# Kernel optimization log

Hardware: AMD Instinct MI355X
Metric: run time of the kernel (lower is better)

Reference implementation:

```python
import jax, jax.numpy as jnp
import numpy as np

N_CHANNELS = 1024
N_HEADS = 16
SEQ = 2048
BATCH = 2


def setup_inputs() -> dict:
    key = jax.random.key(0)
    k1, k2, k3 = jax.random.split(key, 3)
    x = jax.random.normal(k1, (BATCH, SEQ, N_CHANNELS), dtype=jnp.float32)
    qkv_w = jax.random.normal(k2, (3 * N_CHANNELS, N_CHANNELS), dtype=jnp.float32) * 0.02
    qkv_b = jnp.zeros((3 * N_CHANNELS,), dtype=jnp.float32)
    proj_w = jax.random.normal(k3, (N_CHANNELS, N_CHANNELS), dtype=jnp.float32) * 0.02
    proj_b = jnp.zeros((N_CHANNELS,), dtype=jnp.float32)
    return {"x": x, "qkv_w": qkv_w, "qkv_b": qkv_b, "proj_w": proj_w, "proj_b": proj_b}


def reference(x, qkv_w, qkv_b, proj_w, proj_b):
    bs, t, c = x.shape
    h = N_HEADS
    hd = c // h
    scale = hd ** (-0.5)
    # qkv projection: torch Linear is x @ W^T + b
    qkv = x @ qkv_w.T + qkv_b  # [B, T, 3C]
    qkv = qkv.reshape(bs, t, 3, h, hd)
    q, k, v = qkv[:, :, 0], qkv[:, :, 1], qkv[:, :, 2]  # each [B, T, H, hd]
    logits = jnp.einsum('bthc,bshc->bhts', q, k) * scale  # [B, H, T, T]
    # causal mask: log(tril(ones)) -> 0 below diag, -inf above
    causal = jnp.tril(jnp.ones((t, t), dtype=bool))
    logits = jnp.where(causal[None, None], logits, -jnp.inf)
    attn = jax.nn.softmax(logits, axis=-1)
    out = jnp.einsum('bhts,bshc->bthc', attn, v).reshape(bs, t, c)
    out = out @ proj_w.T + proj_b
    return out
```

## Files before the change

### kernel.cpp

```cpp
#include <hip/hip_runtime.h>

typedef __bf16 bf16x8 __attribute__((ext_vector_type(8)));
typedef float f32x4 __attribute__((ext_vector_type(4)));
typedef float f32x16 __attribute__((ext_vector_type(16)));

__device__ inline ushort f2bf(float f) {
    unsigned u = __builtin_bit_cast(unsigned, f);
    unsigned r = (u + 0x7FFFu + ((u >> 16) & 1u)) >> 16;
    return (ushort)r;
}
__device__ inline float bf2f(ushort u) {
    unsigned x = ((unsigned)u) << 16;
    return __builtin_bit_cast(float, x);
}
__device__ inline uint4 pack8(const float* f) {
    uint4 r;
    r.x = (unsigned)f2bf(f[0]) | ((unsigned)f2bf(f[1]) << 16);
    r.y = (unsigned)f2bf(f[2]) | ((unsigned)f2bf(f[3]) << 16);
    r.z = (unsigned)f2bf(f[4]) | ((unsigned)f2bf(f[5]) << 16);
    r.w = (unsigned)f2bf(f[6]) | ((unsigned)f2bf(f[7]) << 16);
    return r;
}
__device__ inline unsigned cvtpk_bf16(float lo, float hi) {
    unsigned r;
    asm("v_cvt_pk_bf16_f32 %0, %1, %2" : "=v"(r) : "v"(lo), "v"(hi));
    return r;
}

#define MFMA_BF16(a, b, c) __builtin_amdgcn_mfma_f32_16x16x32_bf16(a, b, c, 0, 0, 0)
#define MFMA32(a, b, c) __builtin_amdgcn_mfma_f32_32x32x16_bf16(a, b, c, 0, 0, 0)
#define GLDS(g, l) __builtin_amdgcn_global_load_lds( \
    (const __attribute__((address_space(1))) void*)(g), \
    (__attribute__((address_space(3))) void*)(l), 16, 0, 0)

#define QSCALE 0.18033688011112042f

__global__ __launch_bounds__(256) void convert3(
    const float* __restrict__ s0, ushort* __restrict__ d0,
    const float* __restrict__ s1, ushort* __restrict__ d1,
    const float* __restrict__ s2, ushort* __restrict__ d2)
{
    const int i = blockIdx.x * 256 + threadIdx.x;
    const float* s; ushort* d; int off;
    if (i < 524288)      { s = s0; d = d0; off = i; }
    else if (i < 917504) { s = s1; d = d1; off = i - 524288; }
    else                 { s = s2; d = d2; off = i - 917504; }
    const float4* f = (const float4*)s + off * 2;
    float fa[8];
    *(float4*)&fa[0] = f[0];
    *(float4*)&fa[4] = f[1];
    ((uint4*)d)[off] = pack8(fa);
}

__global__ __launch_bounds__(256) void gemm_qkv(
    const ushort* __restrict__ A, const ushort* __restrict__ B,
    const float* __restrict__ bias,
    ushort* __restrict__ outQ, ushort* __restrict__ outK, ushort* __restrict__ outV,
    int N, int K)
{
    __shared__ __align__(16) ushort SMEM[32768];

    const int tid = threadIdx.x;
    const int w = tid >> 6;
    const int lane = tid & 63;
    const int l15 = lane & 15;
    const int quad = lane >> 4;
    const int srow = lane >> 3;

    const int bid = blockIdx.x + (blockIdx.y << 5);
    const int nb = (bid & 7) * 96 + (bid >> 3);
    const int m0 = (nb / 24) * 128;
    const int n0 = (nb % 24) * 128;
    const int wr = (w & 1) * 64;
    const int wc = (w >> 1) * 64;

    auto stage = [&](int k0, int buf) {
        ushort* As = SMEM + buf * 16384;
        ushort* Bs = As + 8192;
#pragma unroll
        for (int j = 0; j < 4; j++) {
            const int r0 = w * 32 + j * 8;
            const int row = r0 + srow;
            const int gcol = ((lane & 7) ^ (row & 7)) * 8;
            GLDS(A + (size_t)(m0 + row) * K + k0 + gcol, As + r0 * 64);
            GLDS(B + (size_t)(n0 + row) * K + k0 + gcol, Bs + r0 * 64);
        }
    };

    f32x4 acc[4][4] = {};

    stage(0, 0);
    __syncthreads();

    for (int k0 = 0; k0 < K; k0 += 64) {
        const int cur = (k0 >> 6) & 1;
        if (k0 + 64 < K) stage(k0 + 64, cur ^ 1);

        const ushort* As = SMEM + cur * 16384;
        const ushort* Bs = As + 8192;
        bf16x8 af[4][2], bf[4][2];
#pragma unroll
        for (int i = 0; i < 4; i++)
#pragma unroll
            for (int kk = 0; kk < 2; kk++) {
                const int ra = wr + i * 16 + l15;
                const int rb = wc + i * 16 + l15;
                af[i][kk] = *(const bf16x8*)&As[ra * 64 + (((kk * 4 + quad) ^ (ra & 7)) * 8)];
                bf[i][kk] = *(const bf16x8*)&Bs[rb * 64 + (((kk * 4 + quad) ^ (rb & 7)) * 8)];
            }
#pragma unroll
        for (int kk = 0; kk < 2; kk++)
#pragma unroll
            for (int mi = 0; mi < 4; mi++)
#pragma unroll
                for (int ni = 0; ni < 4; ni++)
                    acc[mi][ni] = MFMA_BF16(af[mi][kk], bf[ni][kk], acc[mi][ni]);
        __syncthreads();
    }

    const int which = n0 >> 10;
    ushort* Ct = SMEM;
    if (which == 2) {
#pragma unroll
        for (int mi = 0; mi < 4; mi++)
#pragma unroll
            for (int ni = 0; ni < 4; ni++)
#pragma unroll
                for (int r = 0; r < 4; r++) {
                    const int m_loc = wr + mi * 16 + quad * 4 + r;
                    const int n_loc = wc + ni * 16 + l15;
                    Ct[n_loc * 136 + m_loc] =
                        f2bf(acc[mi][ni][r] + bias[n0 + n_loc]);
                }
        __syncthreads();
        const int b = m0 >> 11;
#pragma unroll
        for (int i = 0; i < 8; i++) {
            const int vi = tid + i * 256;
            const int n_loc = vi >> 4, mblk = vi & 15;
            const uint4 val = *(const uint4*)&Ct[n_loc * 136 + mblk * 8];
            const int t = (m0 & 2047) + mblk * 8;
            const int c = (n0 + n_loc) & 1023;
            const int h = c >> 6, d = c & 63;
            *(uint4*)&outV[((size_t)(b * 16 + h) * 64 + d) * 2048 + t] = val;
        }
    } else {
        const float qs = (which == 0) ? QSCALE : 1.0f;
#pragma unroll
        for (int mi = 0; mi < 4; mi++)
#pragma unroll
            for (int ni = 0; ni < 4; ni++)
#pragma unroll
                for (int r = 0; r < 4; r++) {
                    const int m_loc = wr + mi * 16 + quad * 4 + r;
                    const int n_loc = wc + ni * 16 + l15;
                    Ct[m_loc * 136 + n_loc] =
                        f2bf((acc[mi][ni][r] + bias[n0 + n_loc]) * qs);
                }
        __syncthreads();
        ushort* outP = (which == 0) ? outQ : outK;
        const int hb = (n0 & 1023) >> 6;
        const int b = m0 >> 11;
#pragma unroll
        for (int i = 0; i < 8; i++) {
            const int vi = tid + i * 256;
            const int m_loc = vi >> 4, u = vi & 15;
            const uint4 val = *(const uint4*)&Ct[m_loc * 136 + u * 8];
            const int t = (m0 & 2047) + m_loc;
            const int h = hb + (u >> 3);
            const int d8 = (u & 7) * 8;
            *(uint4*)&outP[((size_t)(b * 16 + h)) * 131072 + (size_t)t * 64 + d8] = val;
        }
    }
}

__global__ __launch_bounds__(256) void gemm_proj(
    const ushort* __restrict__ A, const ushort* __restrict__ B,
    const float* __restrict__ bias, float* __restrict__ outD)
{
    const int N = 1024, K = 1024;
    __shared__ __align__(16) ushort SMEM[24576];

    const int tid = threadIdx.x;
    const int w = tid >> 6;
    const int lane = tid & 63;
    const int l15 = lane & 15;
    const int quad = lane >> 4;
    const int srow = lane >> 3;

    const int bid = blockIdx.x + (blockIdx.y << 6);
    const int nb = (bid & 7) * 64 + (bid >> 3);
    const int m0 = (nb >> 3) * 64;
    const int n0 = (nb & 7) * 128;
    const int wr = (w & 1) * 32;
    const int wc = (w >> 1) * 64;

    auto stage = [&](int k0, int buf) {
        ushort* As = SMEM + buf * 12288;
        ushort* Bs = As + 4096;
#pragma unroll
        for (int j = 0; j < 2; j++) {
            const int r0 = w * 16 + j * 8;
            const int row = r0 + srow;
            const int gcol = ((lane & 7) ^ (row & 7)) * 8;
            GLDS(A + (size_t)(m0 + row) * K + k0 + gcol, As + r0 * 64);
        }
#pragma unroll
        for (int j = 0; j < 4; j++) {
            const int r0 = w * 32 + j * 8;
            const int row = r0 + srow;
            const int gcol = ((lane & 7) ^ (row & 7)) * 8;
            GLDS(B + (size_t)(n0 + row) * K + k0 + gcol, Bs + r0 * 64);
        }
    };

    f32x4 acc[2][4] = {};

    stage(0, 0);
    __syncthreads();

    for (int k0 = 0; k0 < K; k0 += 64) {
        const int cur = (k0 >> 6) & 1;
        if (k0 + 64 < K) stage(k0 + 64, cur ^ 1);

        const ushort* As = SMEM + cur * 12288;
        const ushort* Bs = As + 4096;
        bf16x8 af[2][2], bf[4][2];
#pragma unroll
        for (int kk = 0; kk < 2; kk++) {
#pragma unroll
            for (int mi = 0; mi < 2; mi++) {
                const int ra = wr + mi * 16 + l15;
                af[mi][kk] = *(const bf16x8*)&As[ra * 64 + (((kk * 4 + quad) ^ (ra & 7)) * 8)];
            }
#pragma unroll
            for (int ni = 0; ni < 4; ni++) {
                const int rb = wc + ni * 16 + l15;
                bf[ni][kk] = *(const bf16x8*)&Bs[rb * 64 + (((kk * 4 + quad) ^ (rb & 7)) * 8)];
            }
        }
#pragma unroll
        for (int kk = 0; kk < 2; kk++)
#pragma unroll
            for (int mi = 0; mi < 2; mi++)
#pragma unroll
                for (int ni = 0; ni < 4; ni++)
                    acc[mi][ni] = MFMA_BF16(af[mi][kk], bf[ni][kk], acc[mi][ni]);
        __syncthreads();
    }

    float* Cf = (float*)SMEM;
#pragma unroll
    for (int cch = 0; cch < 2; cch++) {
        __syncthreads();
        if ((wc >> 6) == cch) {
#pragma unroll
            for (int mi = 0; mi < 2; mi++)
#pragma unroll
                for (int ni = 0; ni < 4; ni++)
#pragma unroll
                    for (int r = 0; r < 4; r++) {
                        const int m_loc = wr + mi * 16 + quad * 4 + r;
                        const int nl = ni * 16 + l15;
                        Cf[m_loc * 68 + nl] = acc[mi][ni][r] + bias[n0 + cch * 64 + nl];
                    }
        }
        __syncthreads();
#pragma unroll
        for (int i = 0; i < 4; i++) {
            const int vi = tid + i * 256;
            const int m_loc = vi >> 4, u = vi & 15;
            const float4 val = *(const float4*)&Cf[m_loc * 68 + u * 4];
            *(float4*)&outD[(size_t)(m0 + m_loc) * N + n0 + cch * 64 + u * 4] = val;
        }
    }
}

__global__ __launch_bounds__(256, 4) void attn_split(
    const ushort* __restrict__ Q, const ushort* __restrict__ K,
    const ushort* __restrict__ Vt, ushort* __restrict__ O,
    ushort* __restrict__ Opart, float* __restrict__ Lpart)
{
    __shared__ __align__(16) ushort KV[2][2][64 * 64];

    const int bid0 = blockIdx.x + blockIdx.y * 32;
    const int nb = (bid0 & 7) * 160 + (bid0 >> 3);
    const int bh = (nb / 160) * 4 + (nb % 160) / 40;
    const int y = nb % 40;

    int qt, k0, k1, split;
    const int slot = y - 4;
    if (y < 4) {
        qt = y; k0 = 0; k1 = 2 * qt + 2; split = 0;
    } else {
        split = 1;
        const int z = y - 4;
        int ci, c;
        if (z < 8)       { qt = 4 + (z >> 1); ci = z & 1; c = 2; }
        else if (z < 20) { const int t = z - 8;  qt = 8 + t / 3;   ci = t % 3; c = 3; }
        else             { const int t = z - 20; qt = 12 + (t >> 2); ci = t & 3; c = 4; }
        const int n = 2 * qt + 2;
        k0 = ci * n / c;
        k1 = (ci + 1) * n / c;
    }
    const int q0 = qt * 128;
    const int tid = threadIdx.x;
    const int w = tid >> 6;
    const int lane = tid & 63;
    const int l31 = lane & 31;
    const int hf = lane >> 5;
    const int wrow0 = q0 + w * 32;
    const int rowg = wrow0 + l31;

    auto stage = [&](int kt, int b) {
        const int t0 = kt * 64;
#pragma unroll
        for (int j = 0; j < 2; j++) {
            const int r0 = w * 16 + j * 8;
            const int row = r0 + (lane >> 3);
            const int gcol = ((lane & 7) ^ (row & 7)) * 8;
            GLDS(K + ((size_t)bh * 2048 + t0 + row) * 64 + gcol, &KV[b][0][r0 * 64]);
            GLDS(Vt + ((size_t)bh * 64 + row) * 2048 + t0 + gcol, &KV[b][1][r0 * 64]);
        }
    };

    const ushort* qbase = Q + ((size_t)bh * 2048 + rowg) * 64 + hf * 8;
    bf16x8 qf[4];
#pragma unroll
    for (int db = 0; db < 4; db++) qf[db] = *(const bf16x8*)(qbase + db * 16);

    bf16x8 ones;
#pragma unroll
    for (int j = 0; j < 8; j++) ones[j] = (__bf16)1.0f;

    f32x16 oacc[2] = {};
    f32x16 lacc = {};

    stage(k0, 0);

    for (int kt = k0; kt < k1; kt++) {
        __syncthreads();
        if (kt + 1 < k1) stage(kt + 1, (kt + 1 - k0) & 1);

        const ushort* Ks = &KV[(kt - k0) & 1][0][0];
        const ushort* Vs = &KV[(kt - k0) & 1][1][0];
        const int t0 = kt * 64;

        if (t0 <= wrow0 + 31) {
            f32x16 sacc[2] = {};
#pragma unroll
            for (int db = 0; db < 4; db++)
#pragma unroll
                for (int kb = 0; kb < 2; kb++) {
                    const int rr = kb * 32 + l31;
                    bf16x8 kf = *(const bf16x8*)&Ks[rr * 64 + (((db * 2 + hf) ^ (rr & 7)) * 8)];
                    sacc[kb] = MFMA32(kf, qf[db], sacc[kb]);
                }

            unsigned u[2][8];
            const bool nm = (t0 + 63 > wrow0);
#pragma unroll
            for (int kb = 0; kb < 2; kb++) {
                float p[16];
                if (nm) {
#pragma unroll
                    for (int reg = 0; reg < 16; reg++) {
                        const int col = t0 + kb * 32 + (reg & 3) + 8 * (reg >> 2) + 4 * hf;
                        float x = (col > rowg) ? -1e30f : sacc[kb][reg];
                        p[reg] = __builtin_exp2f(x);
                    }
                } else {
#pragma unroll
                    for (int reg = 0; reg < 16; reg++)
                        p[reg] = __builtin_exp2f(sacc[kb][reg]);
                }
#pragma unroll
                for (int t = 0; t < 8; t++)
                    u[kb][t] = cvtpk_bf16(p[2 * t], p[2 * t + 1]);
            }

#pragma unroll
            for (int kb = 0; kb < 2; kb++)
#pragma unroll
                for (int g = 0; g < 4; g++) {
                    const int tp = (g & 1) + (g >> 1) * 4;
                    asm("v_permlane32_swap_b32 %0, %1"
                        : "+v"(u[kb][tp]), "+v"(u[kb][tp + 2]));
                }

#pragma unroll
            for (int m = 0; m < 4; m++) {
                uint4 av;
                av.x = u[m >> 1][(m & 1) * 4 + 0];
                av.y = u[m >> 1][(m & 1) * 4 + 1];
                av.z = u[m >> 1][(m & 1) * 4 + 2];
                av.w = u[m >> 1][(m & 1) * 4 + 3];
                bf16x8 af = __builtin_bit_cast(bf16x8, av);
                lacc = MFMA32(af, ones, lacc);
#pragma unroll
                for (int d2 = 0; d2 < 2; d2++) {
                    const int rr = d2 * 32 + l31;
                    bf16x8 vf = *(const bf16x8*)&Vs[rr * 64 + (((m * 2 + hf) ^ (rr & 7)) * 8)];
                    oacc[d2] = MFMA32(af, vf, oacc[d2]);
                }
            }
        }
    }

    ushort* Ob = &KV[(k1 - k0) & 1][0][0];
    if (split) {
        if (l31 == 0) {
            const size_t slot2 = (size_t)bh * 36 + slot;
#pragma unroll
            for (int reg = 0; reg < 16; reg++)
                Lpart[slot2 * 128 + w * 32 + (reg & 3) + 8 * (reg >> 2) + 4 * hf] = lacc[reg];
        }
#pragma unroll
        for (int reg = 0; reg < 16; reg++) {
            const int rl = w * 32 + (reg & 3) + 8 * (reg >> 2) + 4 * hf;
#pragma unroll
            for (int d2 = 0; d2 < 2; d2++)
                Ob[rl * 64 + d2 * 32 + l31] = f2bf(oacc[d2][reg]);
        }
    } else {
#pragma unroll
        for (int reg = 0; reg < 16; reg++) {
            const float inv = 1.0f / lacc[reg];
            const int rl = w * 32 + (reg & 3) + 8 * (reg >> 2) + 4 * hf;
#pragma unroll
            for (int d2 = 0; d2 < 2; d2++)
                Ob[rl * 64 + d2 * 32 + l31] = f2bf(oacc[d2][reg] * inv);
        }
    }
    __syncthreads();
    if (split) {
        const size_t slot2 = (size_t)bh * 36 + slot;
        ushort* dst = Opart + slot2 * 8192;
#pragma unroll
        for (int i = 0; i < 4; i++) {
            const int idx = tid + i * 256;
            *(uint4*)&dst[idx * 8] = *(const uint4*)&Ob[idx * 8];
        }
    } else {
        const int b = bh >> 4, hh = bh & 15;
#pragma unroll
        for (int i = 0; i < 4; i++) {
            const int idx = tid + i * 256;
            const int rl = idx >> 3, c0 = (idx & 7) * 8;
            *(uint4*)&O[((size_t)b * 2048 + q0 + rl) * 1024 + hh * 64 + c0] =
                *(const uint4*)&Ob[idx * 8];
        }
    }
}

__global__ __launch_bounds__(256) void attn_combine(
    const ushort* __restrict__ Opart, const float* __restrict__ Lpart,
    ushort* __restrict__ O)
{
    const int bh = blockIdx.x;
    const int qt = 4 + blockIdx.y;
    const int c = (qt >> 2) + 1;
    int base;
    if (qt < 8)       base = (qt - 4) * 2;
    else if (qt < 12) base = 8 + (qt - 8) * 3;
    else              base = 20 + (qt - 12) * 4;
    const int tid = threadIdx.x;
    const int row = tid >> 1;
    const int dg = (tid & 1) * 32;
    const size_t s = (size_t)bh * 36 + base;
    float lsum = 0.f;
    for (int j = 0; j < c; j++) lsum += Lpart[(s + j) * 128 + row];
    const float inv = 1.0f / lsum;
    const int b = bh >> 4, hh = bh & 15;
    ushort* dst = O + ((size_t)b * 2048 + qt * 128 + row) * 1024 + hh * 64 + dg;
#pragma unroll
    for (int v = 0; v < 4; v++) {
        float accf[8] = {};
        for (int j = 0; j < c; j++) {
            uint4 a = *(const uint4*)(Opart + (s + j) * 8192 + row * 64 + dg + v * 8);
            const ushort* ua = (const ushort*)&a;
#pragma unroll
            for (int t = 0; t < 8; t++) accf[t] += bf2f(ua[t]);
        }
        ushort out[8];
#pragma unroll
        for (int t = 0; t < 8; t++) out[t] = f2bf(accf[t] * inv);
        *(uint4*)(dst + v * 8) = *(uint4*)out;
    }
}

extern "C" void kernel_launch(void* const* d_in, const int* in_sizes, int n_in,
                              void* d_out, int out_size, void* d_ws, size_t ws_size,
                              hipStream_t stream) {
    const float* x      = (const float*)d_in[0];
    const float* qkv_w  = (const float*)d_in[1];
    const float* qkv_b  = (const float*)d_in[2];
    const float* proj_w = (const float*)d_in[3];
    const float* proj_b = (const float*)d_in[4];

    ushort* XbOb  = (ushort*)d_ws + 16;
    ushort* Wproj = XbOb + 4194304;
    ushort* Qb    = Wproj + 1048576;
    ushort* Kb    = Qb + 4194304;
    ushort* Vt    = Kb + 4194304;
    ushort* Wqkv  = Vt + 4194304;
    ushort* Opart = Wqkv;
    float*  Lpart = (float*)(Opart + 9437184);

    convert3<<<4096, 256, 0, stream>>>(x, XbOb, qkv_w, Wqkv, proj_w, Wproj);
    gemm_qkv<<<dim3(32, 24), 256, 0, stream>>>(XbOb, Wqkv, qkv_b,
                                               Qb, Kb, Vt, 3072, 1024);
    attn_split<<<dim3(32, 40), 256, 0, stream>>>(Qb, Kb, Vt, XbOb, Opart, Lpart);
    attn_combine<<<dim3(32, 12), 256, 0, stream>>>(Opart, Lpart, XbOb);
    gemm_proj<<<dim3(64, 8), 256, 0, stream>>>(XbOb, Wproj, proj_b, (float*)d_out);
}
```

Baseline: 204.3 us.

## Load K/V fragments directly from global memory into registers, drop LDS staging

The attention kernel no longer stages K and V tiles into double-buffered shared memory with async global-to-LDS loads and per-iteration barriers. Each wave now reads its K and V MFMA fragments straight from global memory into registers, and only a small LDS buffer is kept for the output epilogue. Launch bounds drop from 4 to 3 blocks per CU to leave more registers for the fragments. This removes the __syncthreads and LDS traffic, but each wave re-fetches K/V that the block's four waves previously shared, and there is no prefetch to hide global latency.

```diff
diff --git a/kernel.cpp b/kernel.cpp
--- a/kernel.cpp
+++ b/kernel.cpp
@@ -276,12 +276,12 @@
     }
 }
 
-__global__ __launch_bounds__(256, 4) void attn_split(
+__global__ __launch_bounds__(256, 3) void attn_split(
     const ushort* __restrict__ Q, const ushort* __restrict__ K,
     const ushort* __restrict__ Vt, ushort* __restrict__ O,
     ushort* __restrict__ Opart, float* __restrict__ Lpart)
 {
-    __shared__ __align__(16) ushort KV[2][2][64 * 64];
+    __shared__ __align__(16) ushort Ob[128 * 64];
 
     const int bid0 = blockIdx.x + blockIdx.y * 32;
     const int nb = (bid0 & 7) * 160 + (bid0 >> 3);
@@ -312,17 +312,8 @@
     const int wrow0 = q0 + w * 32;
     const int rowg = wrow0 + l31;
 
-    auto stage = [&](int kt, int b) {
-        const int t0 = kt * 64;
-#pragma unroll
-        for (int j = 0; j < 2; j++) {
-            const int r0 = w * 16 + j * 8;
-            const int row = r0 + (lane >> 3);
-            const int gcol = ((lane & 7) ^ (row & 7)) * 8;
-            GLDS(K + ((size_t)bh * 2048 + t0 + row) * 64 + gcol, &KV[b][0][r0 * 64]);
-            GLDS(Vt + ((size_t)bh * 64 + row) * 2048 + t0 + gcol, &KV[b][1][r0 * 64]);
-        }
-    };
+    const ushort* Kb = K + (size_t)bh * 2048 * 64;
+    const ushort* Vb = Vt + (size_t)bh * 64 * 2048;
 
     const ushort* qbase = Q + ((size_t)bh * 2048 + rowg) * 64 + hf * 8;
     bf16x8 qf[4];
@@ -336,78 +327,78 @@
     f32x16 oacc[2] = {};
     f32x16 lacc = {};
 
-    stage(k0, 0);
-
     for (int kt = k0; kt < k1; kt++) {
-        __syncthreads();
-        if (kt + 1 < k1) stage(kt + 1, (kt + 1 - k0) & 1);
-
-        const ushort* Ks = &KV[(kt - k0) & 1][0][0];
-        const ushort* Vs = &KV[(kt - k0) & 1][1][0];
         const int t0 = kt * 64;
-
-        if (t0 <= wrow0 + 31) {
-            f32x16 sacc[2] = {};
-#pragma unroll
-            for (int db = 0; db < 4; db++)
-#pragma unroll
-                for (int kb = 0; kb < 2; kb++) {
-                    const int rr = kb * 32 + l31;
-                    bf16x8 kf = *(const bf16x8*)&Ks[rr * 64 + (((db * 2 + hf) ^ (rr & 7)) * 8)];
-                    sacc[kb] = MFMA32(kf, qf[db], sacc[kb]);
+        if (t0 > wrow0 + 31) continue;
+
+        bf16x8 kv[8];
+#pragma unroll
+        for (int db = 0; db < 4; db++)
+#pragma unroll
+            for (int kb = 0; kb < 2; kb++)
+                kv[db * 2 + kb] = *(const bf16x8*)
+                    &Kb[(size_t)(t0 + kb * 32 + l31) * 64 + (db * 2 + hf) * 8];
+
+        f32x16 sacc[2] = {};
+#pragma unroll
+        for (int db = 0; db < 4; db++)
+#pragma unroll
+            for (int kb = 0; kb < 2; kb++)
+                sacc[kb] = MFMA32(kv[db * 2 + kb], qf[db], sacc[kb]);
+
+        unsigned u[2][8];
+        const bool nm = (t0 + 63 > wrow0);
+#pragma unroll
+        for (int kb = 0; kb < 2; kb++) {
+            float p[16];
+            if (nm) {
+#pragma unroll
+                for (int reg = 0; reg < 16; reg++) {
+                    const int col = t0 + kb * 32 + (reg & 3) + 8 * (reg >> 2) + 4 * hf;
+                    float x = (col > rowg) ? -1e30f : sacc[kb][reg];
+                    p[reg] = __builtin_exp2f(x);
                 }
-
-            unsigned u[2][8];
-            const bool nm = (t0 + 63 > wrow0);
-#pragma unroll
-            for (int kb = 0; kb < 2; kb++) {
-                float p[16];
-                if (nm) {
-#pragma unroll
-                    for (int reg = 0; reg < 16; reg++) {
-                        const int col = t0 + kb * 32 + (reg & 3) + 8 * (reg >> 2) + 4 * hf;
-                        float x = (col > rowg) ? -1e30f : sacc[kb][reg];
-                        p[reg] = __builtin_exp2f(x);
-                    }
-                } else {
-#pragma unroll
-                    for (int reg = 0; reg < 16; reg++)
-                        p[reg] = __builtin_exp2f(sacc[kb][reg]);
-                }
-#pragma unroll
-                for (int t = 0; t < 8; t++)
-                    u[kb][t] = cvtpk_bf16(p[2 * t], p[2 * t + 1]);
+            } else {
+#pragma unroll
+                for (int reg = 0; reg < 16; reg++)
+                    p[reg] = __builtin_exp2f(sacc[kb][reg]);
             }
-
-#pragma unroll
-            for (int kb = 0; kb < 2; kb++)
-#pragma unroll
-                for (int g = 0; g < 4; g++) {
-                    const int tp = (g & 1) + (g >> 1) * 4;
-                    asm("v_permlane32_swap_b32 %0, %1"
-                        : "+v"(u[kb][tp]), "+v"(u[kb][tp + 2]));
-                }
-
-#pragma unroll
-            for (int m = 0; m < 4; m++) {
-                uint4 av;
-                av.x = u[m >> 1][(m & 1) * 4 + 0];
-                av.y = u[m >> 1][(m & 1) * 4 + 1];
-                av.z = u[m >> 1][(m & 1) * 4 + 2];
-                av.w = u[m >> 1][(m & 1) * 4 + 3];
-                bf16x8 af = __builtin_bit_cast(bf16x8, av);
-                lacc = MFMA32(af, ones, lacc);
-#pragma unroll
-                for (int d2 = 0; d2 < 2; d2++) {
-                    const int rr = d2 * 32 + l31;
-                    bf16x8 vf = *(const bf16x8*)&Vs[rr * 64 + (((m * 2 + hf) ^ (rr & 7)) * 8)];
-                    oacc[d2] = MFMA32(af, vf, oacc[d2]);
-                }
+#pragma unroll
+            for (int t = 0; t < 8; t++)
+                u[kb][t] = cvtpk_bf16(p[2 * t], p[2 * t + 1]);
+        }
+
+#pragma unroll
+        for (int m = 0; m < 4; m++)
+#pragma unroll
+            for (int d2 = 0; d2 < 2; d2++)
+                kv[m * 2 + d2] = *(const bf16x8*)
+                    &Vb[(size_t)(d2 * 32 + l31) * 2048 + t0 + (m * 2 + hf) * 8];
+
+#pragma unroll
+        for (int kb = 0; kb < 2; kb++)
+#pragma unroll
+            for (int g = 0; g < 4; g++) {
+                const int tp = (g & 1) + (g >> 1) * 4;
+                asm("v_permlane32_swap_b32 %0, %1"
+                    : "+v"(u[kb][tp]), "+v"(u[kb][tp + 2]));
             }
-        }
-    }
-
-    ushort* Ob = &KV[(k1 - k0) & 1][0][0];
+
+#pragma unroll
+        for (int m = 0; m < 4; m++) {
+            uint4 av;
+            av.x = u[m >> 1][(m & 1) * 4 + 0];
+            av.y = u[m >> 1][(m & 1) * 4 + 1];
+            av.z = u[m >> 1][(m & 1) * 4 + 2];
+            av.w = u[m >> 1][(m & 1) * 4 + 3];
+            bf16x8 af = __builtin_bit_cast(bf16x8, av);
+            lacc = MFMA32(af, ones, lacc);
+#pragma unroll
+            for (int d2 = 0; d2 < 2; d2++)
+                oacc[d2] = MFMA32(af, kv[m * 2 + d2], oacc[d2]);
+        }
+    }
+
     if (split) {
         if (l31 == 0) {
             const size_t slot2 = (size_t)bh * 36 + slot;
```

Measured after the change: 234.9 us. +15.0%, slower.
